# Kernel optimization log

Measured on AMD Instinct MI355X. Metric: run time of the kernel, lower is better.

The kernel has to match this reference:

```python
import jax, jax.numpy as jnp
import numpy as np

LAYERS, BLOCKS = 10, 4
RES_CH, END_CH, CLASSES, GROUPS = 32, 256, 256, 1
BN_EPS = 1e-5


def conv1x1(x, w, b):
    # x: (bn, Cin, L), w: (Cout, Cin), b: (Cout,)
    return jnp.einsum('oc,bcl->bol', w, x) + b[None, :, None]


def mish(x):
    return x * jnp.tanh(jax.nn.softplus(x))


def concat_mish(x):
    return mish(jnp.concatenate((x, -x), axis=1))


def channel_shuffle(x, groups):
    if groups == 1:
        return x
    bn, c, l = x.shape
    return x.reshape(bn, groups, c // groups, l).transpose(0, 2, 1, 3).reshape(bn, c, l)


def batchnorm_train(x, g, b):
    # BatchNorm1d in training mode: per-channel stats over (batch, length), biased var
    m = jnp.mean(x, axis=(0, 2), keepdims=True)
    v = jnp.mean((x - m) ** 2, axis=(0, 2), keepdims=True)
    return (x - m) * jax.lax.rsqrt(v + BN_EPS) * g[None, :, None] + b[None, :, None]


def dilate(x, dilation, init_dilation, pad_start=True):
    bn, c, l = x.shape
    if dilation == 1:
        x = jnp.transpose(x, (1, 2, 0)).reshape(c, l * init_dilation, bn // init_dilation)
        return jnp.transpose(x, (2, 0, 1))
    f = dilation // init_dilation
    if f == 1:
        return x
    new_l = (l + f - 1) // f * f
    if new_l != l:
        pad = (new_l - l, 0) if pad_start else (0, new_l - l)
        x = jnp.pad(x, ((0, 0), (0, 0), pad))
        l = new_l
    l //= f
    bn *= f
    x = jnp.transpose(x, (1, 2, 0)).reshape(c, l, bn)
    return jnp.transpose(x, (2, 0, 1))


def setup_inputs() -> dict:
    key = jax.random.key(0)
    ks = iter(jax.random.split(key, 32))
    nl = LAYERS * BLOCKS
    f32 = jnp.float32
    inp = {
        'x': jax.random.normal(next(ks), (8, CLASSES, 8192), dtype=f32),
        'start_w': jax.random.normal(next(ks), (RES_CH, CLASSES), dtype=f32) * 0.05,
        'start_b': jnp.zeros((RES_CH,), f32),
        'gate_w': jax.random.normal(next(ks), (nl, RES_CH // 2, RES_CH), dtype=f32) * 0.15,
        'gate_b': jnp.zeros((nl, RES_CH // 2), f32),
        'res_w': jax.random.normal(next(ks), (nl, RES_CH, RES_CH), dtype=f32) * 0.15,
        'res_b': jnp.zeros((nl, RES_CH), f32),
        'bn_g': jnp.ones((nl, RES_CH), f32),
        'bn_b': jnp.zeros((nl, RES_CH), f32),
        'end_bn1_g': jnp.ones((RES_CH,), f32),
        'end_bn1_b': jnp.zeros((RES_CH,), f32),
        'end_conv1_w': jax.random.normal(next(ks), (END_CH // 2, 2 * RES_CH), dtype=f32) * 0.1,
        'end_conv1_b': jnp.zeros((END_CH // 2,), f32),
        'end_bn2_g': jnp.ones((END_CH // 2,), f32),
        'end_bn2_b': jnp.zeros((END_CH // 2,), f32),
        'end_conv2_w': jax.random.normal(next(ks), (CLASSES, END_CH), dtype=f32) * 0.05,
        'end_conv2_b': jnp.zeros((CLASSES,), f32),
    }
    return inp


def reference(x, start_w, start_b, gate_w, gate_b, res_w, res_b, bn_g, bn_b,
              end_bn1_g, end_bn1_b, end_conv1_w, end_conv1_b,
              end_bn2_g, end_bn2_b, end_conv2_w, end_conv2_b):
    x = conv1x1(x, start_w, start_b)
    prev_dilation = 1
    i = 0
    for block in range(BLOCKS):
        for layer in range(LAYERS):
            x = dilate(x, 2 ** layer, prev_dilation)
            prev_dilation = 2 ** layer
            x0 = x
            h = concat_mish(conv1x1(x, gate_w[i], gate_b[i]))
            h = channel_shuffle(h, GROUPS)
            h = batchnorm_train(conv1x1(h, res_w[i], res_b[i]), bn_g[i], bn_b[i])
            h = channel_shuffle(h, GROUPS)
            x = x0 + h
            i += 1
    x = concat_mish(batchnorm_train(x, end_bn1_g, end_bn1_b))
    x = concat_mish(batchnorm_train(conv1x1(x, end_conv1_w, end_conv1_b), end_bn2_g, end_bn2_b))
    x = conv1x1(x, end_conv2_w, end_conv2_b)
    x = dilate(x, 1, 2 ** (LAYERS - 1))
    return x
```

## Files before the change

kernel.cpp:

```cpp
#include <hip/hip_runtime.h>

#define BS 256
#define STATS_F   0
#define W2T_F     46080
#define XBUF_F    131072
#define RBUF_F    2228224
#define WS_NEED_BYTES (4325376ull * 4ull)

__device__ __forceinline__ void mish2(float v, float& mp, float& mn) {
  float vc = fminf(fmaxf(v, -30.f), 30.f);
  float u  = __expf(vc);
  float n1 = u * (u + 2.f);
  mp = v * n1 * __builtin_amdgcn_rcpf(n1 + 2.f);
  float n2 = fmaf(2.f, u, 1.f);
  float d2 = fmaf(2.f * u, u, n2);
  mn = -v * n2 * __builtin_amdgcn_rcpf(d2);
}

__device__ __forceinline__ void block_reduce_stats(const float (&vals)[32],
    float* s_red, float* s_p2, float* slot, int t) {
  #pragma unroll
  for (int cc = 0; cc < 8; ++cc) {
    float4 v = make_float4(vals[cc*4+0], vals[cc*4+1], vals[cc*4+2], vals[cc*4+3]);
    *(float4*)(&s_red[t*32 + ((cc ^ (t & 7)) << 2)]) = v;
  }
  __syncthreads();
  {
    int q = t & 63, grp = t >> 6, c = q & 31;
    bool issq = (q >= 32);
    float acc = 0.f;
    #pragma clang loop unroll_count(8)
    for (int rr = 0; rr < 64; ++rr) {
      int row = grp * 64 + rr;
      float v = s_red[row*32 + ((((c >> 2) ^ (row & 7)) << 2) | (c & 3))];
      acc = fmaf(v, issq ? v : 1.f, acc);
    }
    s_p2[t] = acc;
  }
  __syncthreads();
  if (t < 64) {
    float tot = s_p2[t] + s_p2[t+64] + s_p2[t+128] + s_p2[t+192];
    unsafeAtomicAdd(&slot[(blockIdx.x & 15) * 64 + t], tot);
  }
  __syncthreads();
}

__device__ __forceinline__ void bn32_from_slot(const float* slot, const float* g,
    const float* b, float* sA, float* sB, float* s_tmp, int t) {
  if (t < 64) {
    float s = 0.f;
    #pragma unroll
    for (int rep = 0; rep < 16; ++rep) s += slot[rep*64 + t];
    s_tmp[t] = s;
  }
  __syncthreads();
  if (t < 32) {
    float mean = s_tmp[t] * (1.f/65536.f);
    float var  = fmaf(-mean, mean, s_tmp[t+32] * (1.f/65536.f));
    float sc   = g[t] * rsqrtf(var + 1e-5f);
    sA[t] = sc;
    sB[t] = fmaf(-mean, sc, b[t]);
  }
  __syncthreads();
}

__device__ __forceinline__ void layer_convs(const float (&x)[32], float (&r)[32],
    const float* gw, const float* gb, const float* rw, const float* rb, int i) {
  float g[16];
  #pragma unroll
  for (int j = 0; j < 16; ++j) g[j] = gb[i*16 + j];
  #pragma unroll
  for (int j = 0; j < 16; ++j)
    #pragma unroll
    for (int k = 0; k < 32; ++k)
      g[j] = fmaf(gw[i*512 + j*32 + k], x[k], g[j]);
  float cm[32];
  #pragma unroll
  for (int j = 0; j < 16; ++j) mish2(g[j], cm[j], cm[j+16]);
  #pragma unroll
  for (int j = 0; j < 32; ++j) r[j] = rb[i*32 + j];
  #pragma unroll
  for (int j = 0; j < 32; ++j)
    #pragma unroll
    for (int k = 0; k < 32; ++k)
      r[j] = fmaf(rw[i*1024 + j*32 + k], cm[k], r[j]);
}

__device__ __forceinline__ void layer_convs_lds(const float (&x)[32], float (&r)[32],
    const float* wg, const float* gbv, const float* wrs, const float* rbv) {
  float g[16];
  #pragma unroll
  for (int j = 0; j < 16; ++j) g[j] = gbv[j];
  #pragma unroll
  for (int j = 0; j < 16; ++j) {
    const float4* w = (const float4*)&wg[j*32];
    #pragma unroll
    for (int k4 = 0; k4 < 8; ++k4) {
      float4 a = w[k4];
      g[j] = fmaf(a.x, x[k4*4+0], g[j]);
      g[j] = fmaf(a.y, x[k4*4+1], g[j]);
      g[j] = fmaf(a.z, x[k4*4+2], g[j]);
      g[j] = fmaf(a.w, x[k4*4+3], g[j]);
    }
  }
  float cm[32];
  #pragma unroll
  for (int j = 0; j < 16; ++j) mish2(g[j], cm[j], cm[j+16]);
  #pragma unroll
  for (int j = 0; j < 32; ++j) r[j] = rbv[j];
  #pragma unroll
  for (int j = 0; j < 32; ++j) {
    const float4* w = (const float4*)&wrs[j*32];
    #pragma unroll
    for (int k4 = 0; k4 < 8; ++k4) {
      float4 a = w[k4];
      r[j] = fmaf(a.x, cm[k4*4+0], r[j]);
      r[j] = fmaf(a.y, cm[k4*4+1], r[j]);
      r[j] = fmaf(a.z, cm[k4*4+2], r[j]);
      r[j] = fmaf(a.w, cm[k4*4+3], r[j]);
    }
  }
}

__global__ void __launch_bounds__(BS) k_start(const float* __restrict__ xin,
    const float* __restrict__ sw, const float* __restrict__ sb,
    const float* __restrict__ gw, const float* __restrict__ gb,
    const float* __restrict__ rw, const float* __restrict__ rb,
    const float* __restrict__ c2w, float* __restrict__ ws) {
  __shared__ float s_red[BS*32];
  __shared__ float s_p2[BS];
  __shared__ float s_w[1536];
  int t = threadIdx.x, p = blockIdx.x * BS + t;
  float* w2t = ws + W2T_F; float* xb = ws + XBUF_F; float* rbf = ws + RBUF_F;
  float* s_sw = s_red;
  {
    const float4* s4 = (const float4*)sw;
    float4* d4 = (float4*)s_sw;
    #pragma unroll
    for (int q = 0; q < 8; ++q) d4[q*BS + t] = s4[q*BS + t];
    if (t < 128) ((float4*)s_w)[t] = ((const float4*)gw)[t];
    ((float4*)(s_w + 512))[t] = ((const float4*)rw)[t];
  }
  { int o = p & 255, kk = p >> 8; w2t[kk*256 + o] = c2w[o*256 + kk]; }
  __syncthreads();
  int bb = p >> 13, ll = p & 8191;
  int pbase = bb * 2097152 + ll;
  float x[32];
  #pragma unroll
  for (int j = 0; j < 32; ++j) x[j] = sb[j];
  #pragma clang loop unroll(disable)
  for (int c8 = 0; c8 < 32; ++c8) {
    float xv[8];
    #pragma unroll
    for (int cc = 0; cc < 8; ++cc) xv[cc] = xin[pbase + (c8*8+cc)*8192];
    #pragma unroll
    for (int j = 0; j < 32; ++j)
      #pragma unroll
      for (int cc = 0; cc < 8; ++cc)
        x[j] = fmaf(s_sw[j*256 + c8*8 + cc], xv[cc], x[j]);
  }
  float r[32];
  layer_convs_lds(x, r, s_w, gb, s_w + 512, rb);
  #pragma unroll
  for (int c = 0; c < 32; ++c) { xb[c*65536 + p] = x[c]; rbf[c*65536 + p] = r[c]; }
  __syncthreads();
  block_reduce_stats(r, s_red, s_p2, ws + STATS_F, t);
}

__global__ void __launch_bounds__(BS) k_layer(const float* __restrict__ gw,
    const float* __restrict__ gb, const float* __restrict__ rw,
    const float* __restrict__ rb, const float* __restrict__ bng,
    const float* __restrict__ bnb, float* __restrict__ ws, int i) {
  __shared__ float s_red[BS*32];
  __shared__ float s_p2[BS];
  __shared__ float s_A[32], s_B[32], s_tmp[64];
  __shared__ float s_w[1536];
  int t = threadIdx.x, p = blockIdx.x * BS + t;
  float* stats = ws + STATS_F; float* xb = ws + XBUF_F; float* rbf = ws + RBUF_F;
  if (t < 128) ((float4*)s_w)[t] = ((const float4*)(gw + i*512))[t];
  ((float4*)(s_w + 512))[t] = ((const float4*)(rw + i*1024))[t];
  bn32_from_slot(stats + (i-1)*1024, bng + (i-1)*32, bnb + (i-1)*32, s_A, s_B, s_tmp, t);
  float x[32], r[32];
  #pragma unroll
  for (int c = 0; c < 32; ++c) { x[c] = xb[c*65536 + p]; r[c] = rbf[c*65536 + p]; }
  #pragma unroll
  for (int c = 0; c < 32; ++c) x[c] += fmaf(r[c], s_A[c], s_B[c]);
  float rn[32];
  layer_convs_lds(x, rn, s_w, gb + i*16, s_w + 512, rb + i*32);
  #pragma unroll
  for (int c = 0; c < 32; ++c) { xb[c*65536 + p] = x[c]; rbf[c*65536 + p] = rn[c]; }
  block_reduce_stats(rn, s_red, s_p2, stats + i*1024, t);
}

__global__ void __launch_bounds__(BS) k_end1(const float* __restrict__ bng,
    const float* __restrict__ bnb, float* __restrict__ ws) {
  __shared__ float s_red[BS*32];
  __shared__ float s_p2[BS];
  __shared__ float s_A[32], s_B[32], s_tmp[64];
  int t = threadIdx.x, p = blockIdx.x * BS + t;
  float* stats = ws + STATS_F; float* xb = ws + XBUF_F; float* rbf = ws + RBUF_F;
  bn32_from_slot(stats + 39*1024, bng + 39*32, bnb + 39*32, s_A, s_B, s_tmp, t);
  float x[32];
  #pragma unroll
  for (int c = 0; c < 32; ++c) {
    float r = rbf[c*65536 + p];
    x[c] = xb[c*65536 + p] + fmaf(r, s_A[c], s_B[c]);
    xb[c*65536 + p] = x[c];
  }
  block_reduce_stats(x, s_red, s_p2, stats + 40*1024, t);
}

__global__ void __launch_bounds__(BS) k_end2(const float* __restrict__ e1g,
    const float* __restrict__ e1b, const float* __restrict__ c1w,
    const float* __restrict__ c1b, float* __restrict__ ws) {
  __shared__ float s_red[BS*32];
  __shared__ float s_p2[BS];
  __shared__ float s_A[32], s_B[32], s_tmp[64];
  __shared__ float s_c1wp[2048];
  __shared__ float s_c1b[128];
  int t = threadIdx.x, p = blockIdx.x * BS + t;
  float* stats = ws + STATS_F; float* xb = ws + XBUF_F;
  if (t < 32) ((float4*)s_c1b)[t] = ((const float4*)c1b)[t];
  bn32_from_slot(stats + 40*1024, e1g, e1b, s_A, s_B, s_tmp, t);
  float mp[32], mn[32];
  #pragma unroll
  for (int c = 0; c < 32; ++c) {
    float xh = fmaf(xb[c*65536 + p], s_A[c], s_B[c]);
    mish2(xh, mp[c], mn[c]);
  }
  #pragma clang loop unroll(disable)
  for (int pp = 0; pp < 4; ++pp) {
    { const float4* s = (const float4*)(c1w + pp*2048);
      float4* d = (float4*)s_c1wp;
      d[t] = s[t]; d[256 + t] = s[256 + t]; }
    __syncthreads();
    float zc[32];
    #pragma unroll
    for (int j = 0; j < 32; ++j) zc[j] = s_c1b[pp*32 + j];
    #pragma unroll
    for (int j = 0; j < 32; ++j) {
      const float4* cw = (const float4*)&s_c1wp[j*64];
      #pragma unroll
      for (int k4 = 0; k4 < 8; ++k4) {
        float4 a = cw[k4], b = cw[8+k4];
        zc[j] = fmaf(a.x, mp[k4*4+0], zc[j]);
        zc[j] = fmaf(a.y, mp[k4*4+1], zc[j]);
        zc[j] = fmaf(a.z, mp[k4*4+2], zc[j]);
        zc[j] = fmaf(a.w, mp[k4*4+3], zc[j]);
        zc[j] = fmaf(b.x, mn[k4*4+0], zc[j]);
        zc[j] = fmaf(b.y, mn[k4*4+1], zc[j]);
        zc[j] = fmaf(b.z, mn[k4*4+2], zc[j]);
        zc[j] = fmaf(b.w, mn[k4*4+3], zc[j]);
      }
    }
    block_reduce_stats(zc, s_red, s_p2, stats + (41+pp)*1024, t);
  }
}

__global__ void __launch_bounds__(BS) k_end3(const float* __restrict__ e1g,
    const float* __restrict__ e1b, const float* __restrict__ c1w,
    const float* __restrict__ c1b, const float* __restrict__ e2g,
    const float* __restrict__ e2b, const float* __restrict__ c2b,
    float* __restrict__ out, float* __restrict__ ws) {
  __shared__ float s_A[32], s_B[32], s_tmp[64];
  __shared__ float s_A2[128], s_B2[128];
  __shared__ float s_c1w[8192];
  __shared__ float s_c1b[128];
  __shared__ float s_c2b[64];
  __shared__ float4 wbuf[64][16];
  int t = threadIdx.x, p = blockIdx.x * BS + t;
  float* stats = ws + STATS_F; float* xb = ws + XBUF_F; float* w2t = ws + W2T_F;
  const int ocb = blockIdx.y * 64;
  const int wr = t >> 2, wc = t & 3;
  { float4* d = (float4*)s_c1w; const float4* s = (const float4*)c1w;
    #pragma unroll
    for (int q = 0; q < 8; ++q) d[q*BS + t] = s[q*BS + t]; }
  if (t < 32) ((float4*)s_c1b)[t] = ((const float4*)c1b)[t];
  else if (t < 48) ((float4*)s_c2b)[t-32] = ((const float4*)(c2b + ocb))[t-32];
  { int kr = (wr < 32) ? wr : (wr + 96);
    const float4* s = (const float4*)(w2t + kr*256 + ocb) + wc*4;
    float4* d = &wbuf[wr][wc*4];
    d[0] = s[0]; d[1] = s[1]; d[2] = s[2]; d[3] = s[3]; }
  bn32_from_slot(stats + 40*1024, e1g, e1b, s_A, s_B, s_tmp, t);
  if (t < 128) {
    int pp = t >> 5, c = t & 31;
    const float* sl = stats + (41+pp)*1024;
    float S = 0.f, Q = 0.f;
    #pragma unroll
    for (int rep = 0; rep < 16; ++rep) { S += sl[rep*64 + c]; Q += sl[rep*64 + 32 + c]; }
    float mean = S * (1.f/65536.f);
    float var  = fmaf(-mean, mean, Q * (1.f/65536.f));
    float sc   = e2g[t] * rsqrtf(var + 1e-5f);
    s_A2[t] = sc;
    s_B2[t] = fmaf(-mean, sc, e2b[t]);
  }
  __syncthreads();
  float mp[32], mn[32];
  #pragma unroll
  for (int c = 0; c < 32; ++c) {
    float xh = fmaf(xb[c*65536 + p], s_A[c], s_B[c]);
    mish2(xh, mp[c], mn[c]);
  }
  float acc[64];
  #pragma unroll
  for (int o = 0; o < 64; ++o) acc[o] = s_c2b[o];
  #pragma clang loop unroll(disable)
  for (int kc = 0; kc < 4; ++kc) {
    float4 pa, pb, pc, pd;
    if (kc < 3) {
      int kr = (wr < 32) ? ((kc+1)*32 + wr) : ((kc+1)*32 + wr + 96);
      const float4* s = (const float4*)(w2t + kr*256 + ocb) + wc*4;
      pa = s[0]; pb = s[1]; pc = s[2]; pd = s[3];
    }
    #pragma clang loop unroll_count(2)
    for (int j = 0; j < 32; ++j) {
      const int k = kc*32 + j;
      float z = s_c1b[k];
      const float4* cw = (const float4*)&s_c1w[k*64];
      #pragma unroll
      for (int k4 = 0; k4 < 8; ++k4) {
        float4 a = cw[k4], b = cw[8+k4];
        z = fmaf(a.x, mp[k4*4+0], z);
        z = fmaf(a.y, mp[k4*4+1], z);
        z = fmaf(a.z, mp[k4*4+2], z);
        z = fmaf(a.w, mp[k4*4+3], z);
        z = fmaf(b.x, mn[k4*4+0], z);
        z = fmaf(b.y, mn[k4*4+1], z);
        z = fmaf(b.z, mn[k4*4+2], z);
        z = fmaf(b.w, mn[k4*4+3], z);
      }
      float zh = fmaf(z, s_A2[k], s_B2[k]);
      float mpv, mnv; mish2(zh, mpv, mnv);
      const float4* w0 = wbuf[j];
      const float4* w1 = wbuf[32 + j];
      #pragma unroll
      for (int o4 = 0; o4 < 16; ++o4) {
        float4 a = w0[o4], b = w1[o4];
        acc[o4*4+0] = fmaf(a.x, mpv, fmaf(b.x, mnv, acc[o4*4+0]));
        acc[o4*4+1] = fmaf(a.y, mpv, fmaf(b.y, mnv, acc[o4*4+1]));
        acc[o4*4+2] = fmaf(a.z, mpv, fmaf(b.z, mnv, acc[o4*4+2]));
        acc[o4*4+3] = fmaf(a.w, mpv, fmaf(b.w, mnv, acc[o4*4+3]));
      }
    }
    if (kc < 3) {
      __syncthreads();
      float4* d = &wbuf[wr][wc*4];
      d[0] = pa; d[1] = pb; d[2] = pc; d[3] = pd;
      __syncthreads();
    }
  }
  int bb = p >> 13, ll = p & 8191;
  int obase = bb * 2097152 + ocb * 8192 + ll;
  #pragma unroll
  for (int o = 0; o < 64; ++o) out[obase + o*8192] = acc[o];
}

#define NBLK 256
#define CNTS_U  4096
#define W2T_FB  4608
#define STATS_OUT_OFF (8u*1024u*1024u)
#define SLOT_STRIDE 16384

__device__ __forceinline__ float coherent_ld(const float* p) {
  return __hip_atomic_load(p, __ATOMIC_RELAXED, __HIP_MEMORY_SCOPE_AGENT);
}
__device__ __forceinline__ void coherent_st(float* p, float v) {
  __hip_atomic_store(p, v, __ATOMIC_RELAXED, __HIP_MEMORY_SCOPE_AGENT);
}
__device__ __forceinline__ void grid_sync_fb(float* ws, unsigned gen, bool flush) {
  __syncthreads();
  unsigned* flags = (unsigned*)ws;
  unsigned* cnts  = (unsigned*)ws + CNTS_U;
  if (blockIdx.x == 0) {
    if (threadIdx.x == 0) {
      if (flush) __threadfence();
      __hip_atomic_fetch_add(&cnts[0], 1u, __ATOMIC_RELAXED, __HIP_MEMORY_SCOPE_AGENT);
      unsigned sum;
      do {
        __builtin_amdgcn_s_sleep(2);
        sum = 0;
        #pragma unroll
        for (int x = 0; x < 32; ++x)
          sum += __hip_atomic_load(&cnts[x*16], __ATOMIC_RELAXED, __HIP_MEMORY_SCOPE_AGENT);
      } while (sum < gen * NBLK);
    }
    __syncthreads();
    __hip_atomic_store(&flags[threadIdx.x * 16], gen,
                       __ATOMIC_RELAXED, __HIP_MEMORY_SCOPE_AGENT);
  } else {
    if (threadIdx.x == 0) {
      if (flush) __threadfence();
      __hip_atomic_fetch_add(&cnts[(blockIdx.x & 31) * 16], 1u,
                             __ATOMIC_RELAXED, __HIP_MEMORY_SCOPE_AGENT);
      while (__hip_atomic_load(&flags[blockIdx.x * 16],
                               __ATOMIC_RELAXED, __HIP_MEMORY_SCOPE_AGENT) < gen)
        __builtin_amdgcn_s_sleep(2);
    }
    __syncthreads();
  }
}
__device__ __forceinline__ void brs_fb(const float (&vals)[32],
    float* s_red, float* s_p2, float* slot, int t) {
  #pragma unroll
  for (int cc = 0; cc < 8; ++cc) {
    float4 v = make_float4(vals[cc*4+0], vals[cc*4+1], vals[cc*4+2], vals[cc*4+3]);
    *(float4*)(&s_red[t*32 + ((cc ^ (t & 7)) << 2)]) = v;
  }
  __syncthreads();
  {
    int q = t & 63, grp = t >> 6, c = q & 31;
    bool issq = (q >= 32);
    float acc = 0.f;
    #pragma clang loop unroll_count(8)
    for (int rr = 0; rr < 64; ++rr) {
      int row = grp * 64 + rr;
      float v = s_red[row*32 + ((((c >> 2) ^ (row & 7)) << 2) | (c & 3))];
      acc = fmaf(v, issq ? v : 1.f, acc);
    }
    s_p2[t] = acc;
  }
  __syncthreads();
  if (t < 64) {
    float tot = s_p2[t] + s_p2[t+64] + s_p2[t+128] + s_p2[t+192];
    coherent_st(&slot[blockIdx.x * 64 + t], tot);
  }
}

extern "C" __global__ void __launch_bounds__(BS, 1)
qnet_fb(const float* __restrict__ xin,
        const float* __restrict__ sw, const float* __restrict__ sb,
        const float* __restrict__ gw, const float* __restrict__ gb,
        const float* __restrict__ rw, const float* __restrict__ rb,
        const float* __restrict__ bng, const float* __restrict__ bnb,
        const float* __restrict__ e1g, const float* __restrict__ e1b,
        const float* __restrict__ c1w, const float* __restrict__ c1b,
        const float* __restrict__ e2g, const float* __restrict__ e2b,
        const float* __restrict__ c2w, const float* __restrict__ c2b,
        float* __restrict__ out, float* __restrict__ ws)
{
  __shared__ float s_red[BS*32];
  __shared__ float s_p2[BS];
  __shared__ float s_tot[64];
  __shared__ float s_bcA[128];
  __shared__ float s_bcB[128];
  const int t = threadIdx.x;
  const int p = blockIdx.x * BS + t;
  float* w2t = ws + W2T_FB;
  float* zg  = out;
  float* sg  = out + STATS_OUT_OFF;
  unsigned gen = 0;
  const int bb = p >> 13, ll = p & 8191;
  const int pbase = bb * 2097152 + ll;
  { int o = p & 255, kk = p >> 8; coherent_st(&w2t[kk*256 + o], c2w[o*256 + kk]); }
  float x[32];
  #pragma unroll
  for (int j = 0; j < 32; ++j) x[j] = sb[j];
  #pragma clang loop unroll(disable)
  for (int c8 = 0; c8 < 32; ++c8) {
    float xv[8];
    #pragma unroll
    for (int cc = 0; cc < 8; ++cc) xv[cc] = xin[pbase + (c8*8+cc)*8192];
    #pragma unroll
    for (int j = 0; j < 32; ++j)
      #pragma unroll
      for (int cc = 0; cc < 8; ++cc)
        x[j] = fmaf(sw[j*256 + c8*8 + cc], xv[cc], x[j]);
  }
  #pragma clang loop unroll(disable)
  for (int i = 0; i < 40; ++i) {
    float r[32];
    layer_convs(x, r, gw, gb, rw, rb, i);
    brs_fb(r, s_red, s_p2, sg + (size_t)i * SLOT_STRIDE, t);
    ++gen; grid_sync_fb(ws, gen, false);
    {
      int q = t & 63, w = t >> 6;
      const float* col = sg + (size_t)i * SLOT_STRIDE + q;
      float acc2 = 0.f;
      #pragma clang loop unroll_count(16)
      for (int j = 0; j < 64; ++j) acc2 += coherent_ld(&col[(w*64+j)*64]);
      s_p2[t] = acc2;
    }
    __syncthreads();
    if (t < 64) s_tot[t] = s_p2[t] + s_p2[t+64] + s_p2[t+128] + s_p2[t+192];
    __syncthreads();
    if (t < 32) {
      float mean = s_tot[t] * (1.f/65536.f);
      float var  = fmaf(-mean, mean, s_tot[t+32] * (1.f/65536.f));
      float sc   = bng[i*32+t] * rsqrtf(var + 1e-5f);
      s_bcA[t] = sc;
      s_bcB[t] = fmaf(-mean, sc, bnb[i*32+t]);
    }
    __syncthreads();
    #pragma unroll
    for (int c = 0; c < 32; ++c) x[c] += fmaf(r[c], s_bcA[c], s_bcB[c]);
  }
  brs_fb(x, s_red, s_p2, sg + 40 * SLOT_STRIDE, t);
  ++gen; grid_sync_fb(ws, gen, false);
  {
    int q = t & 63, w = t >> 6;
    const float* col = sg + (size_t)40 * SLOT_STRIDE + q;
    float acc2 = 0.f;
    #pragma clang loop unroll_count(16)
    for (int j = 0; j < 64; ++j) acc2 += coherent_ld(&col[(w*64+j)*64]);
    s_p2[t] = acc2;
  }
  __syncthreads();
  if (t < 64) s_tot[t] = s_p2[t] + s_p2[t+64] + s_p2[t+128] + s_p2[t+192];
  __syncthreads();
  if (t < 32) {
    float mean = s_tot[t] * (1.f/65536.f);
    float var  = fmaf(-mean, mean, s_tot[t+32] * (1.f/65536.f));
    float sc   = e1g[t] * rsqrtf(var + 1e-5f);
    s_bcA[t] = sc;
    s_bcB[t] = fmaf(-mean, sc, e1b[t]);
  }
  __syncthreads();
  float mp[32], mn[32];
  #pragma unroll
  for (int c = 0; c < 32; ++c) {
    float xh = fmaf(x[c], s_bcA[c], s_bcB[c]);
    mish2(xh, mp[c], mn[c]);
  }
  #pragma clang loop unroll(disable)
  for (int pp = 0; pp < 4; ++pp) {
    float zc[32];
    #pragma unroll
    for (int j = 0; j < 32; ++j) zc[j] = c1b[pp*32 + j];
    #pragma unroll
    for (int j = 0; j < 32; ++j)
      #pragma unroll
      for (int k = 0; k < 32; ++k) {
        zc[j] = fmaf(c1w[(pp*32+j)*64 + k],      mp[k], zc[j]);
        zc[j] = fmaf(c1w[(pp*32+j)*64 + 32 + k], mn[k], zc[j]);
      }
    #pragma unroll
    for (int j = 0; j < 32; ++j) zg[(pp*32+j)*65536 + p] = zc[j];
    brs_fb(zc, s_red, s_p2, sg + (size_t)(41+pp) * SLOT_STRIDE, t);
    __syncthreads();
  }
  ++gen; grid_sync_fb(ws, gen, false);
  {
    int slot = 41 + (t >> 6), q = t & 63;
    const float* col = sg + (size_t)slot * SLOT_STRIDE + q;
    float acc2 = 0.f;
    #pragma clang loop unroll_count(32)
    for (int b2 = 0; b2 < 256; ++b2) acc2 += coherent_ld(&col[b2*64]);
    s_p2[t] = acc2;
  }
  __syncthreads();
  if (t < 128) {
    float S = s_p2[((t>>5)<<6) | (t&31)];
    float Q = s_p2[((t>>5)<<6) | 32 | (t&31)];
    float mean = S * (1.f/65536.f);
    float var  = fmaf(-mean, mean, Q * (1.f/65536.f));
    float sc   = e2g[t] * rsqrtf(var + 1e-5f);
    s_bcA[t] = sc;
    s_bcB[t] = fmaf(-mean, sc, e2b[t]);
  }
  __syncthreads();
  float acc[256];
  #pragma unroll
  for (int o = 0; o < 256; ++o) acc[o] = c2b[o];
  float zv_next = zg[p];
  #pragma clang loop unroll(disable)
  for (int k = 0; k < 128; ++k) {
    float zv = zv_next;
    zv_next = zg[((k+1)&127)*65536 + p];
    float zh = fmaf(zv, s_bcA[k], s_bcB[k]);
    float mpv, mnv; mish2(zh, mpv, mnv);
    const float* w0 = &w2t[k*256];
    const float* w1 = &w2t[(k+128)*256];
    #pragma unroll
    for (int o = 0; o < 256; ++o)
      acc[o] = fmaf(w0[o], mpv, fmaf(w1[o], mnv, acc[o]));
  }
  ++gen; grid_sync_fb(ws, gen, true);
  #pragma unroll
  for (int o = 0; o < 256; ++o)
    out[bb*2097152 + o*8192 + ll] = acc[o];
}

extern "C" void kernel_launch(void* const* d_in, const int* in_sizes, int n_in,
                              void* d_out, int out_size, void* d_ws, size_t ws_size,
                              hipStream_t stream) {
  const float* xin = (const float*)d_in[0];
  const float* sw  = (const float*)d_in[1];
  const float* sb  = (const float*)d_in[2];
  const float* gw  = (const float*)d_in[3];
  const float* gb  = (const float*)d_in[4];
  const float* rw  = (const float*)d_in[5];
  const float* rb  = (const float*)d_in[6];
  const float* bng = (const float*)d_in[7];
  const float* bnb = (const float*)d_in[8];
  const float* e1g = (const float*)d_in[9];
  const float* e1b = (const float*)d_in[10];
  const float* c1w = (const float*)d_in[11];
  const float* c1b = (const float*)d_in[12];
  const float* e2g = (const float*)d_in[13];
  const float* e2b = (const float*)d_in[14];
  const float* c2w = (const float*)d_in[15];
  const float* c2b = (const float*)d_in[16];
  float* out = (float*)d_out;
  float* ws  = (float*)d_ws;

  if (ws_size >= WS_NEED_BYTES) {
    hipMemsetAsync(d_ws, 0, 45 * 1024 * 4, stream);
    k_start<<<256, BS, 0, stream>>>(xin, sw, sb, gw, gb, rw, rb, c2w, ws);
    for (int i = 1; i < 40; ++i)
      k_layer<<<256, BS, 0, stream>>>(gw, gb, rw, rb, bng, bnb, ws, i);
    k_end1<<<256, BS, 0, stream>>>(bng, bnb, ws);
    k_end2<<<256, BS, 0, stream>>>(e1g, e1b, c1w, c1b, ws);
    k_end3<<<dim3(256, 4), BS, 0, stream>>>(e1g, e1b, c1w, c1b, e2g, e2b, c2b, out, ws);
  } else {
    hipMemsetAsync(d_ws, 0, (CNTS_U + 512) * 4, stream);
    void* args[] = { &xin, &sw, &sb, &gw, &gb, &rw, &rb, &bng, &bnb,
                     &e1g, &e1b, &c1w, &c1b, &e2g, &e2b, &c2w, &c2b, &out, &ws };
    hipError_t err = hipLaunchCooperativeKernel((const void*)qnet_fb,
                                                dim3(NBLK), dim3(BS), args, 0, stream);
    if (err != hipSuccess) {
      hipLaunchKernelGGL(qnet_fb, dim3(NBLK), dim3(BS), 0, stream,
                         xin, sw, sb, gw, gb, rw, rb, bng, bnb,
                         e1g, e1b, c1w, c1b, e2g, e2b, c2w, c2b, out, ws);
    }
  }
}
```

Before: 1.354 ms.

## Use 128-thread blocks for layer kernels, hoist loads, restage end3 weights

Layer, end1 and end2 kernels now launch 512 blocks of 128 threads instead of 256 blocks of 256, so more blocks spread across the 256 CUs. The block stats reduction is templated on thread count to match. Global loads of x and r are moved ahead of the BN-stat gathering so their latency overlaps that work. k_end3 no longer holds the full conv1 weight in LDS and drops its register prefetch of the second-stage weights. It instead reloads a per-chunk slice of both weights each iteration, which cuts LDS use but adds synchronisation and load stalls.

```diff
diff --git a/kernel.cpp b/kernel.cpp
--- a/kernel.cpp
+++ b/kernel.cpp
@@ -1,6 +1,7 @@
 #include <hip/hip_runtime.h>
 
-#define BS 256
+#define BS  256
+#define BSL 128
 #define STATS_F   0
 #define W2T_F     46080
 #define XBUF_F    131072
@@ -17,6 +18,7 @@
   mn = -v * n2 * __builtin_amdgcn_rcpf(d2);
 }
 
+template<int NT>
 __device__ __forceinline__ void block_reduce_stats(const float (&vals)[32],
     float* s_red, float* s_p2, float* slot, int t) {
   #pragma unroll
@@ -39,7 +41,9 @@
   }
   __syncthreads();
   if (t < 64) {
-    float tot = s_p2[t] + s_p2[t+64] + s_p2[t+128] + s_p2[t+192];
+    float tot = 0.f;
+    #pragma unroll
+    for (int g = 0; g < NT/64; ++g) tot += s_p2[t + g*64];
     unsafeAtomicAdd(&slot[(blockIdx.x & 15) * 64 + t], tot);
   }
   __syncthreads();
@@ -164,75 +168,81 @@
   #pragma unroll
   for (int c = 0; c < 32; ++c) { xb[c*65536 + p] = x[c]; rbf[c*65536 + p] = r[c]; }
   __syncthreads();
-  block_reduce_stats(r, s_red, s_p2, ws + STATS_F, t);
-}
-
-__global__ void __launch_bounds__(BS) k_layer(const float* __restrict__ gw,
+  block_reduce_stats<BS>(r, s_red, s_p2, ws + STATS_F, t);
+}
+
+__global__ void __launch_bounds__(BSL) k_layer(const float* __restrict__ gw,
     const float* __restrict__ gb, const float* __restrict__ rw,
     const float* __restrict__ rb, const float* __restrict__ bng,
     const float* __restrict__ bnb, float* __restrict__ ws, int i) {
-  __shared__ float s_red[BS*32];
-  __shared__ float s_p2[BS];
+  __shared__ float s_red[BSL*32];
+  __shared__ float s_p2[BSL];
   __shared__ float s_A[32], s_B[32], s_tmp[64];
   __shared__ float s_w[1536];
-  int t = threadIdx.x, p = blockIdx.x * BS + t;
+  int t = threadIdx.x, p = blockIdx.x * BSL + t;
   float* stats = ws + STATS_F; float* xb = ws + XBUF_F; float* rbf = ws + RBUF_F;
-  if (t < 128) ((float4*)s_w)[t] = ((const float4*)(gw + i*512))[t];
+  float x[32], r[32];
+  #pragma unroll
+  for (int c = 0; c < 32; ++c) { x[c] = xb[c*65536 + p]; r[c] = rbf[c*65536 + p]; }
+  ((float4*)s_w)[t] = ((const float4*)(gw + i*512))[t];
   ((float4*)(s_w + 512))[t] = ((const float4*)(rw + i*1024))[t];
+  ((float4*)(s_w + 512))[t + 128] = ((const float4*)(rw + i*1024))[t + 128];
   bn32_from_slot(stats + (i-1)*1024, bng + (i-1)*32, bnb + (i-1)*32, s_A, s_B, s_tmp, t);
-  float x[32], r[32];
-  #pragma unroll
-  for (int c = 0; c < 32; ++c) { x[c] = xb[c*65536 + p]; r[c] = rbf[c*65536 + p]; }
   #pragma unroll
   for (int c = 0; c < 32; ++c) x[c] += fmaf(r[c], s_A[c], s_B[c]);
   float rn[32];
   layer_convs_lds(x, rn, s_w, gb + i*16, s_w + 512, rb + i*32);
   #pragma unroll
   for (int c = 0; c < 32; ++c) { xb[c*65536 + p] = x[c]; rbf[c*65536 + p] = rn[c]; }
-  block_reduce_stats(rn, s_red, s_p2, stats + i*1024, t);
-}
-
-__global__ void __launch_bounds__(BS) k_end1(const float* __restrict__ bng,
+  block_reduce_stats<BSL>(rn, s_red, s_p2, stats + i*1024, t);
+}
+
+__global__ void __launch_bounds__(BSL) k_end1(const float* __restrict__ bng,
     const float* __restrict__ bnb, float* __restrict__ ws) {
-  __shared__ float s_red[BS*32];
-  __shared__ float s_p2[BS];
+  __shared__ float s_red[BSL*32];
+  __shared__ float s_p2[BSL];
   __shared__ float s_A[32], s_B[32], s_tmp[64];
-  int t = threadIdx.x, p = blockIdx.x * BS + t;
+  int t = threadIdx.x, p = blockIdx.x * BSL + t;
   float* stats = ws + STATS_F; float* xb = ws + XBUF_F; float* rbf = ws + RBUF_F;
+  float x[32], r[32];
+  #pragma unroll
+  for (int c = 0; c < 32; ++c) { x[c] = xb[c*65536 + p]; r[c] = rbf[c*65536 + p]; }
   bn32_from_slot(stats + 39*1024, bng + 39*32, bnb + 39*32, s_A, s_B, s_tmp, t);
-  float x[32];
   #pragma unroll
   for (int c = 0; c < 32; ++c) {
-    float r = rbf[c*65536 + p];
-    x[c] = xb[c*65536 + p] + fmaf(r, s_A[c], s_B[c]);
+    x[c] += fmaf(r[c], s_A[c], s_B[c]);
     xb[c*65536 + p] = x[c];
   }
-  block_reduce_stats(x, s_red, s_p2, stats + 40*1024, t);
-}
-
-__global__ void __launch_bounds__(BS) k_end2(const float* __restrict__ e1g,
+  block_reduce_stats<BSL>(x, s_red, s_p2, stats + 40*1024, t);
+}
+
+__global__ void __launch_bounds__(BSL) k_end2(const float* __restrict__ e1g,
     const float* __restrict__ e1b, const float* __restrict__ c1w,
     const float* __restrict__ c1b, float* __restrict__ ws) {
-  __shared__ float s_red[BS*32];
-  __shared__ float s_p2[BS];
+  __shared__ float s_red[BSL*32];
+  __shared__ float s_p2[BSL];
   __shared__ float s_A[32], s_B[32], s_tmp[64];
   __shared__ float s_c1wp[2048];
   __shared__ float s_c1b[128];
-  int t = threadIdx.x, p = blockIdx.x * BS + t;
+  int t = threadIdx.x, p = blockIdx.x * BSL + t;
   float* stats = ws + STATS_F; float* xb = ws + XBUF_F;
+  float xv[32];
+  #pragma unroll
+  for (int c = 0; c < 32; ++c) xv[c] = xb[c*65536 + p];
   if (t < 32) ((float4*)s_c1b)[t] = ((const float4*)c1b)[t];
   bn32_from_slot(stats + 40*1024, e1g, e1b, s_A, s_B, s_tmp, t);
   float mp[32], mn[32];
   #pragma unroll
   for (int c = 0; c < 32; ++c) {
-    float xh = fmaf(xb[c*65536 + p], s_A[c], s_B[c]);
+    float xh = fmaf(xv[c], s_A[c], s_B[c]);
     mish2(xh, mp[c], mn[c]);
   }
   #pragma clang loop unroll(disable)
   for (int pp = 0; pp < 4; ++pp) {
     { const float4* s = (const float4*)(c1w + pp*2048);
       float4* d = (float4*)s_c1wp;
-      d[t] = s[t]; d[256 + t] = s[256 + t]; }
+      #pragma unroll
+      for (int q = 0; q < 4; ++q) d[q*BSL + t] = s[q*BSL + t]; }
     __syncthreads();
     float zc[32];
     #pragma unroll
@@ -253,7 +263,7 @@
         zc[j] = fmaf(b.w, mn[k4*4+3], zc[j]);
       }
     }
-    block_reduce_stats(zc, s_red, s_p2, stats + (41+pp)*1024, t);
+    block_reduce_stats<BSL>(zc, s_red, s_p2, stats + (41+pp)*1024, t);
   }
 }
 
@@ -264,23 +274,16 @@
     float* __restrict__ out, float* __restrict__ ws) {
   __shared__ float s_A[32], s_B[32], s_tmp[64];
   __shared__ float s_A2[128], s_B2[128];
-  __shared__ float s_c1w[8192];
+  __shared__ float s_ck[2048];
+  __shared__ float4 wbuf4[1024];
   __shared__ float s_c1b[128];
   __shared__ float s_c2b[64];
-  __shared__ float4 wbuf[64][16];
   int t = threadIdx.x, p = blockIdx.x * BS + t;
-  float* stats = ws + STATS_F; float* xb = ws + XBUF_F; float* w2t = ws + W2T_F;
+  float* stats = ws + STATS_F; float* xb = ws + XBUF_F;
+  const float* w2t = ws + W2T_F;
   const int ocb = blockIdx.y * 64;
-  const int wr = t >> 2, wc = t & 3;
-  { float4* d = (float4*)s_c1w; const float4* s = (const float4*)c1w;
-    #pragma unroll
-    for (int q = 0; q < 8; ++q) d[q*BS + t] = s[q*BS + t]; }
   if (t < 32) ((float4*)s_c1b)[t] = ((const float4*)c1b)[t];
   else if (t < 48) ((float4*)s_c2b)[t-32] = ((const float4*)(c2b + ocb))[t-32];
-  { int kr = (wr < 32) ? wr : (wr + 96);
-    const float4* s = (const float4*)(w2t + kr*256 + ocb) + wc*4;
-    float4* d = &wbuf[wr][wc*4];
-    d[0] = s[0]; d[1] = s[1]; d[2] = s[2]; d[3] = s[3]; }
   bn32_from_slot(stats + 40*1024, e1g, e1b, s_A, s_B, s_tmp, t);
   if (t < 128) {
     int pp = t >> 5, c = t & 31;
@@ -306,17 +309,23 @@
   for (int o = 0; o < 64; ++o) acc[o] = s_c2b[o];
   #pragma clang loop unroll(disable)
   for (int kc = 0; kc < 4; ++kc) {
-    float4 pa, pb, pc, pd;
-    if (kc < 3) {
-      int kr = (wr < 32) ? ((kc+1)*32 + wr) : ((kc+1)*32 + wr + 96);
-      const float4* s = (const float4*)(w2t + kr*256 + ocb) + wc*4;
-      pa = s[0]; pb = s[1]; pc = s[2]; pd = s[3];
-    }
+    __syncthreads();
+    { const float4* cs = (const float4*)(c1w + kc*2048);
+      ((float4*)s_ck)[t]       = cs[t];
+      ((float4*)s_ck)[256 + t] = cs[256 + t]; }
+    #pragma unroll
+    for (int q = 0; q < 4; ++q) {
+      int f = q*256 + t;
+      int r = f >> 4, o4 = f & 15;
+      int kglob = (r < 32) ? (kc*32 + r) : (96 + kc*32 + r);
+      wbuf4[f] = *((const float4*)(w2t + kglob*256 + ocb) + o4);
+    }
+    __syncthreads();
     #pragma clang loop unroll_count(2)
     for (int j = 0; j < 32; ++j) {
       const int k = kc*32 + j;
       float z = s_c1b[k];
-      const float4* cw = (const float4*)&s_c1w[k*64];
+      const float4* cw = (const float4*)&s_ck[j*64];
       #pragma unroll
       for (int k4 = 0; k4 < 8; ++k4) {
         float4 a = cw[k4], b = cw[8+k4];
@@ -331,8 +340,8 @@
       }
       float zh = fmaf(z, s_A2[k], s_B2[k]);
       float mpv, mnv; mish2(zh, mpv, mnv);
-      const float4* w0 = wbuf[j];
-      const float4* w1 = wbuf[32 + j];
+      const float4* w0 = &wbuf4[j*16];
+      const float4* w1 = &wbuf4[(32 + j)*16];
       #pragma unroll
       for (int o4 = 0; o4 < 16; ++o4) {
         float4 a = w0[o4], b = w1[o4];
@@ -341,12 +350,6 @@
         acc[o4*4+2] = fmaf(a.z, mpv, fmaf(b.z, mnv, acc[o4*4+2]));
         acc[o4*4+3] = fmaf(a.w, mpv, fmaf(b.w, mnv, acc[o4*4+3]));
       }
-    }
-    if (kc < 3) {
-      __syncthreads();
-      float4* d = &wbuf[wr][wc*4];
-      d[0] = pa; d[1] = pb; d[2] = pc; d[3] = pd;
-      __syncthreads();
     }
   }
   int bb = p >> 13, ll = p & 8191;
@@ -607,9 +610,9 @@
     hipMemsetAsync(d_ws, 0, 45 * 1024 * 4, stream);
     k_start<<<256, BS, 0, stream>>>(xin, sw, sb, gw, gb, rw, rb, c2w, ws);
     for (int i = 1; i < 40; ++i)
-      k_layer<<<256, BS, 0, stream>>>(gw, gb, rw, rb, bng, bnb, ws, i);
-    k_end1<<<256, BS, 0, stream>>>(bng, bnb, ws);
-    k_end2<<<256, BS, 0, stream>>>(e1g, e1b, c1w, c1b, ws);
+      k_layer<<<512, BSL, 0, stream>>>(gw, gb, rw, rb, bng, bnb, ws, i);
+    k_end1<<<512, BSL, 0, stream>>>(bng, bnb, ws);
+    k_end2<<<512, BSL, 0, stream>>>(e1g, e1b, c1w, c1b, ws);
     k_end3<<<dim3(256, 4), BS, 0, stream>>>(e1g, e1b, c1w, c1b, e2g, e2b, c2b, out, ws);
   } else {
     hipMemsetAsync(d_ws, 0, (CNTS_U + 512) * 4, stream);
```

Result: no change. 1.360 ms (+0.5%).

## Broadcast end-conv2 weights via readlane and chunk end-conv1 weights in LDS

Applied to the files above, without the earlier changes.

In the final end-stage kernel, the conv2 weights are no longer staged through an LDS double buffer. Each lane loads one float4 slice of the row from global memory, and the values are broadcast to the whole wave with readlane into scalar registers. The conv1 weight table now goes into LDS in 32-row chunks per k-step instead of all at once. This cuts LDS footprint and LDS read traffic, which could allow more resident blocks. In exchange it adds per-iteration global loads, readlane and VALU-to-SGPR dependencies, and two barriers per chunk.

```diff
diff --git a/kernel.cpp b/kernel.cpp
--- a/kernel.cpp
+++ b/kernel.cpp
@@ -264,23 +264,16 @@
     float* __restrict__ out, float* __restrict__ ws) {
   __shared__ float s_A[32], s_B[32], s_tmp[64];
   __shared__ float s_A2[128], s_B2[128];
-  __shared__ float s_c1w[8192];
+  __shared__ float s_ck[2048];
   __shared__ float s_c1b[128];
   __shared__ float s_c2b[64];
-  __shared__ float4 wbuf[64][16];
   int t = threadIdx.x, p = blockIdx.x * BS + t;
-  float* stats = ws + STATS_F; float* xb = ws + XBUF_F; float* w2t = ws + W2T_F;
+  float* stats = ws + STATS_F; float* xb = ws + XBUF_F;
+  const float* w2t = ws + W2T_F;
   const int ocb = blockIdx.y * 64;
-  const int wr = t >> 2, wc = t & 3;
-  { float4* d = (float4*)s_c1w; const float4* s = (const float4*)c1w;
-    #pragma unroll
-    for (int q = 0; q < 8; ++q) d[q*BS + t] = s[q*BS + t]; }
+  const int lane15 = t & 15;
   if (t < 32) ((float4*)s_c1b)[t] = ((const float4*)c1b)[t];
   else if (t < 48) ((float4*)s_c2b)[t-32] = ((const float4*)(c2b + ocb))[t-32];
-  { int kr = (wr < 32) ? wr : (wr + 96);
-    const float4* s = (const float4*)(w2t + kr*256 + ocb) + wc*4;
-    float4* d = &wbuf[wr][wc*4];
-    d[0] = s[0]; d[1] = s[1]; d[2] = s[2]; d[3] = s[3]; }
   bn32_from_slot(stats + 40*1024, e1g, e1b, s_A, s_B, s_tmp, t);
   if (t < 128) {
     int pp = t >> 5, c = t & 31;
@@ -306,17 +299,18 @@
   for (int o = 0; o < 64; ++o) acc[o] = s_c2b[o];
   #pragma clang loop unroll(disable)
   for (int kc = 0; kc < 4; ++kc) {
-    float4 pa, pb, pc, pd;
-    if (kc < 3) {
-      int kr = (wr < 32) ? ((kc+1)*32 + wr) : ((kc+1)*32 + wr + 96);
-      const float4* s = (const float4*)(w2t + kr*256 + ocb) + wc*4;
-      pa = s[0]; pb = s[1]; pc = s[2]; pd = s[3];
-    }
+    __syncthreads();
+    { const float4* cs = (const float4*)(c1w + kc*2048);
+      ((float4*)s_ck)[t]       = cs[t];
+      ((float4*)s_ck)[256 + t] = cs[256 + t]; }
+    __syncthreads();
     #pragma clang loop unroll_count(2)
     for (int j = 0; j < 32; ++j) {
       const int k = kc*32 + j;
+      const float4 wv0 = *((const float4*)(w2t + k*256 + ocb) + lane15);
+      const float4 wv1 = *((const float4*)(w2t + (k+128)*256 + ocb) + lane15);
       float z = s_c1b[k];
-      const float4* cw = (const float4*)&s_c1w[k*64];
+      const float4* cw = (const float4*)&s_ck[j*64];
       #pragma unroll
       for (int k4 = 0; k4 < 8; ++k4) {
         float4 a = cw[k4], b = cw[8+k4];
@@ -331,22 +325,21 @@
       }
       float zh = fmaf(z, s_A2[k], s_B2[k]);
       float mpv, mnv; mish2(zh, mpv, mnv);
-      const float4* w0 = wbuf[j];
-      const float4* w1 = wbuf[32 + j];
       #pragma unroll
       for (int o4 = 0; o4 < 16; ++o4) {
-        float4 a = w0[o4], b = w1[o4];
-        acc[o4*4+0] = fmaf(a.x, mpv, fmaf(b.x, mnv, acc[o4*4+0]));
-        acc[o4*4+1] = fmaf(a.y, mpv, fmaf(b.y, mnv, acc[o4*4+1]));
-        acc[o4*4+2] = fmaf(a.z, mpv, fmaf(b.z, mnv, acc[o4*4+2]));
-        acc[o4*4+3] = fmaf(a.w, mpv, fmaf(b.w, mnv, acc[o4*4+3]));
+        float a0 = __int_as_float(__builtin_amdgcn_readlane(__float_as_int(wv0.x), o4));
+        float a1 = __int_as_float(__builtin_amdgcn_readlane(__float_as_int(wv0.y), o4));
+        float a2 = __int_as_float(__builtin_amdgcn_readlane(__float_as_int(wv0.z), o4));
+        float a3 = __int_as_float(__builtin_amdgcn_readlane(__float_as_int(wv0.w), o4));
+        float b0 = __int_as_float(__builtin_amdgcn_readlane(__float_as_int(wv1.x), o4));
+        float b1 = __int_as_float(__builtin_amdgcn_readlane(__float_as_int(wv1.y), o4));
+        float b2 = __int_as_float(__builtin_amdgcn_readlane(__float_as_int(wv1.z), o4));
+        float b3 = __int_as_float(__builtin_amdgcn_readlane(__float_as_int(wv1.w), o4));
+        acc[o4*4+0] = fmaf(a0, mpv, fmaf(b0, mnv, acc[o4*4+0]));
+        acc[o4*4+1] = fmaf(a1, mpv, fmaf(b1, mnv, acc[o4*4+1]));
+        acc[o4*4+2] = fmaf(a2, mpv, fmaf(b2, mnv, acc[o4*4+2]));
+        acc[o4*4+3] = fmaf(a3, mpv, fmaf(b3, mnv, acc[o4*4+3]));
       }
-    }
-    if (kc < 3) {
-      __syncthreads();
-      float4* d = &wbuf[wr][wc*4];
-      d[0] = pa; d[1] = pb; d[2] = pc; d[3] = pd;
-      __syncthreads();
     }
   }
   int bb = p >> 13, ll = p & 8191;
```

Result: slower. 1.412 ms (+4.3%).
